# Kernel optimization log

Hardware: AMD Instinct MI355X
Metric: run time of the kernel (lower is better)

The kernel has to match this reference:

```python
import jax, jax.numpy as jnp
import numpy as np

B, C = 8192, 10000
POS_RATE = 0.005  # ~50 positives per row on average


def setup_inputs() -> dict:
    key = jax.random.key(0)
    k1, k2, k3 = jax.random.split(key, 3)
    output = jax.random.normal(k1, (B, C), dtype=jnp.float32)
    # sparse binary multilabels, guaranteed >=1 positive per row
    ml = (jax.random.uniform(k2, (B, C)) < POS_RATE).astype(jnp.float32)
    gt = jax.random.randint(k3, (B,), 0, C)  # guaranteed ground-truth label per row
    ml = ml.at[jnp.arange(B), gt].set(1.0)
    return {"output": output, "multilabels": ml}


def reference(output, multilabels):
    # Original torch code log_softmaxes `output`, then feeds the result to
    # F.cross_entropy which applies log_softmax AGAIN -> double log_softmax.
    o = jax.nn.log_softmax(output, axis=1)
    o2 = jax.nn.log_softmax(o, axis=1)
    # per-sample loss = min over targets t of -o2[i, t] = -max over targets of o2[i, t]
    neg_inf = jnp.float32(-jnp.inf)
    masked = jnp.where(multilabels == 1.0, o2, neg_inf)
    per_sample = -jnp.max(masked, axis=1)
    return jnp.mean(per_sample)
```

## Files before the change

kernel.cpp:

```cpp
#include <hip/hip_runtime.h>
#include <math.h>

#define NROWS 8192
#define NCOLS 10000
#define NVEC  (NCOLS / 4)
#define NSLOTS 64
#define SLOT_STRIDE 16

typedef float vfloat4 __attribute__((ext_vector_type(4)));

__global__ void zero_ws_kernel(float* ws) {
    ws[threadIdx.x * SLOT_STRIDE] = 0.0f;
}

__global__ __launch_bounds__(256) void min_ce_kernel(
    const float* __restrict__ output,
    const float* __restrict__ ml,
    float* __restrict__ ws)
{
    const int row = blockIdx.x;
    const vfloat4* __restrict__ orow = (const vfloat4*)(output + (size_t)row * NCOLS);
    const vfloat4* __restrict__ mrow = (const vfloat4*)(ml + (size_t)row * NCOLS);

    const float L2E = 1.4426950408889634f;
    float s0 = 0.f, s1 = 0.f, s2 = 0.f, s3 = 0.f;
    float mp = -INFINITY;

    #pragma unroll 4
    for (int i = threadIdx.x; i < NVEC; i += 256) {
        vfloat4 x = __builtin_nontemporal_load(&orow[i]);
        vfloat4 t = __builtin_nontemporal_load(&mrow[i]);

        s0 += __builtin_amdgcn_exp2f(__builtin_fmaf(x.x, L2E, -8.0f));
        s1 += __builtin_amdgcn_exp2f(__builtin_fmaf(x.y, L2E, -8.0f));
        s2 += __builtin_amdgcn_exp2f(__builtin_fmaf(x.z, L2E, -8.0f));
        s3 += __builtin_amdgcn_exp2f(__builtin_fmaf(x.w, L2E, -8.0f));

        mp = fmaxf(mp, t.x == 1.0f ? x.x : -INFINITY);
        mp = fmaxf(mp, t.y == 1.0f ? x.y : -INFINITY);
        mp = fmaxf(mp, t.z == 1.0f ? x.z : -INFINITY);
        mp = fmaxf(mp, t.w == 1.0f ? x.w : -INFINITY);
    }

    float s = (s0 + s1) + (s2 + s3);

    #pragma unroll
    for (int off = 32; off >= 1; off >>= 1) {
        s += __shfl_xor(s, off);
        mp = fmaxf(mp, __shfl_xor(mp, off));
    }

    __shared__ float ss[4], smp[4];
    const int wave = threadIdx.x >> 6;
    const int lane = threadIdx.x & 63;
    if (lane == 0) { ss[wave] = s; smp[wave] = mp; }
    __syncthreads();

    if (threadIdx.x == 0) {
        float S  = (ss[0] + ss[1]) + (ss[2] + ss[3]);
        float MP = fmaxf(fmaxf(smp[0], smp[1]), fmaxf(smp[2], smp[3]));
        float loss = 0.69314718055994531f * (__log2f(S) + 8.0f) - MP;
        atomicAdd(&ws[(row & (NSLOTS - 1)) * SLOT_STRIDE], loss * (1.0f / (float)NROWS));
    }
}

__global__ void final_reduce_kernel(const float* __restrict__ ws, float* __restrict__ out) {
    float v = ws[threadIdx.x * SLOT_STRIDE];
    #pragma unroll
    for (int off = 32; off >= 1; off >>= 1) v += __shfl_xor(v, off);
    if (threadIdx.x == 0) out[0] = v;
}

extern "C" void kernel_launch(void* const* d_in, const int* in_sizes, int n_in,
                              void* d_out, int out_size, void* d_ws, size_t ws_size,
                              hipStream_t stream) {
    const float* output = (const float*)d_in[0];
    const float* ml     = (const float*)d_in[1];
    float* out = (float*)d_out;
    float* ws  = (float*)d_ws;

    zero_ws_kernel<<<1, NSLOTS, 0, stream>>>(ws);
    min_ce_kernel<<<NROWS, 256, 0, stream>>>(output, ml, ws);
    final_reduce_kernel<<<1, 64, 0, stream>>>(ws, out);
}
```

Measured before the change: 574.3 us.

## Map one wavefront per row and drop atomics and the zeroing kernel

Each 64-lane wave now handles a whole row, with four rows per block, so the block-level shared-memory reduction and __syncthreads are gone. Per-row losses are written to a workspace array and summed by a wider final reduction kernel, which replaces the slot atomics and the separate zeroing launch. Splitting the masked max into four independent accumulators shortens the dependency chain. The cost is that each wave runs a longer serial loop per row, which depends on memory-level parallelism to stay hidden.

```diff
diff --git a/kernel.cpp b/kernel.cpp
--- a/kernel.cpp
+++ b/kernel.cpp
@@ -4,30 +4,29 @@
 #define NROWS 8192
 #define NCOLS 10000
 #define NVEC  (NCOLS / 4)
-#define NSLOTS 64
-#define SLOT_STRIDE 16
+#define ROWS_PER_BLOCK 4
+#define NBLOCKS (NROWS / ROWS_PER_BLOCK)
 
 typedef float vfloat4 __attribute__((ext_vector_type(4)));
-
-__global__ void zero_ws_kernel(float* ws) {
-    ws[threadIdx.x * SLOT_STRIDE] = 0.0f;
-}
 
 __global__ __launch_bounds__(256) void min_ce_kernel(
     const float* __restrict__ output,
     const float* __restrict__ ml,
     float* __restrict__ ws)
 {
-    const int row = blockIdx.x;
+    const int wave = threadIdx.x >> 6;
+    const int lane = threadIdx.x & 63;
+    const int row  = blockIdx.x * ROWS_PER_BLOCK + wave;
+
     const vfloat4* __restrict__ orow = (const vfloat4*)(output + (size_t)row * NCOLS);
-    const vfloat4* __restrict__ mrow = (const vfloat4*)(ml + (size_t)row * NCOLS);
+    const vfloat4* __restrict__ mrow = (const vfloat4*)(ml     + (size_t)row * NCOLS);
 
     const float L2E = 1.4426950408889634f;
     float s0 = 0.f, s1 = 0.f, s2 = 0.f, s3 = 0.f;
-    float mp = -INFINITY;
+    float m0 = -INFINITY, m1 = -INFINITY, m2 = -INFINITY, m3 = -INFINITY;
 
     #pragma unroll 4
-    for (int i = threadIdx.x; i < NVEC; i += 256) {
+    for (int i = lane; i < NVEC; i += 64) {
         vfloat4 x = __builtin_nontemporal_load(&orow[i]);
         vfloat4 t = __builtin_nontemporal_load(&mrow[i]);
 
@@ -36,13 +35,14 @@
         s2 += __builtin_amdgcn_exp2f(__builtin_fmaf(x.z, L2E, -8.0f));
         s3 += __builtin_amdgcn_exp2f(__builtin_fmaf(x.w, L2E, -8.0f));
 
-        mp = fmaxf(mp, t.x == 1.0f ? x.x : -INFINITY);
-        mp = fmaxf(mp, t.y == 1.0f ? x.y : -INFINITY);
-        mp = fmaxf(mp, t.z == 1.0f ? x.z : -INFINITY);
-        mp = fmaxf(mp, t.w == 1.0f ? x.w : -INFINITY);
+        m0 = fmaxf(m0, t.x == 1.0f ? x.x : -INFINITY);
+        m1 = fmaxf(m1, t.y == 1.0f ? x.y : -INFINITY);
+        m2 = fmaxf(m2, t.z == 1.0f ? x.z : -INFINITY);
+        m3 = fmaxf(m3, t.w == 1.0f ? x.w : -INFINITY);
     }
 
-    float s = (s0 + s1) + (s2 + s3);
+    float s  = (s0 + s1) + (s2 + s3);
+    float mp = fmaxf(fmaxf(m0, m1), fmaxf(m2, m3));
 
     #pragma unroll
     for (int off = 32; off >= 1; off >>= 1) {
@@ -50,25 +50,31 @@
         mp = fmaxf(mp, __shfl_xor(mp, off));
     }
 
-    __shared__ float ss[4], smp[4];
-    const int wave = threadIdx.x >> 6;
-    const int lane = threadIdx.x & 63;
-    if (lane == 0) { ss[wave] = s; smp[wave] = mp; }
-    __syncthreads();
-
-    if (threadIdx.x == 0) {
-        float S  = (ss[0] + ss[1]) + (ss[2] + ss[3]);
-        float MP = fmaxf(fmaxf(smp[0], smp[1]), fmaxf(smp[2], smp[3]));
-        float loss = 0.69314718055994531f * (__log2f(S) + 8.0f) - MP;
-        atomicAdd(&ws[(row & (NSLOTS - 1)) * SLOT_STRIDE], loss * (1.0f / (float)NROWS));
+    if (lane == 0) {
+        float loss = 0.69314718055994531f * (__log2f(s) + 8.0f) - mp;
+        ws[row] = loss * (1.0f / (float)NROWS);
     }
 }
 
-__global__ void final_reduce_kernel(const float* __restrict__ ws, float* __restrict__ out) {
-    float v = ws[threadIdx.x * SLOT_STRIDE];
+__global__ __launch_bounds__(256) void final_reduce_kernel(
+    const float* __restrict__ ws, float* __restrict__ out)
+{
+    const vfloat4* __restrict__ w4 = (const vfloat4*)ws;
+    float v = 0.f;
+    #pragma unroll
+    for (int i = threadIdx.x; i < NROWS / 4; i += 256) {
+        vfloat4 x = w4[i];
+        v += (x.x + x.y) + (x.z + x.w);
+    }
     #pragma unroll
     for (int off = 32; off >= 1; off >>= 1) v += __shfl_xor(v, off);
-    if (threadIdx.x == 0) out[0] = v;
+
+    __shared__ float sv[4];
+    const int wave = threadIdx.x >> 6;
+    const int lane = threadIdx.x & 63;
+    if (lane == 0) sv[wave] = v;
+    __syncthreads();
+    if (threadIdx.x == 0) out[0] = (sv[0] + sv[1]) + (sv[2] + sv[3]);
 }
 
 extern "C" void kernel_launch(void* const* d_in, const int* in_sizes, int n_in,
@@ -79,7 +85,6 @@
     float* out = (float*)d_out;
     float* ws  = (float*)d_ws;
 
-    zero_ws_kernel<<<1, NSLOTS, 0, stream>>>(ws);
-    min_ce_kernel<<<NROWS, 256, 0, stream>>>(output, ml, ws);
-    final_reduce_kernel<<<1, 64, 0, stream>>>(ws, out);
+    min_ce_kernel<<<NBLOCKS, 256, 0, stream>>>(output, ml, ws);
+    final_reduce_kernel<<<1, 256, 0, stream>>>(ws, out);
 }
```

Measured after the change: 574.1 us. No clear change (-0.0%).
